# Kernel optimization log

Hardware: AMD Instinct MI355X
Metric: run time of the kernel (lower is better)

## Reference

```python
import jax, jax.numpy as jnp
import numpy as np

B, T, H = 8, 1024, 640
N_PHONE, N_PHONEME = 230, 96


def _make_mapping():
    # 0/1 phone->phoneme allophone map, shape (n_phoneme, n_phone).
    # Every phone maps to >=1 phoneme; every phoneme covered (n_phone > n_phoneme).
    rng = np.random.default_rng(0)
    m = np.zeros((N_PHONEME, N_PHONE), dtype=np.float32)
    cols = np.arange(N_PHONE)
    m[cols % N_PHONEME, cols] = 1.0
    m[rng.integers(0, N_PHONEME, size=N_PHONE), cols] = 1.0  # some phones are allophones of 2 phonemes
    m[0, 0] = 1.0  # blank -> blank, as in allophone_layer
    return jnp.asarray(m)


def setup_inputs() -> dict:
    key = jax.random.key(0)
    k1, k2 = jax.random.split(key)
    enc_output = jax.random.normal(k1, (B, T, H), dtype=jnp.float32)
    feature2phone = jax.random.normal(k2, (H, N_PHONE), dtype=jnp.float32)
    return {"enc_output": enc_output, "feature2phone": feature2phone, "mapping": _make_mapping()}


def reference(enc_output, feature2phone, mapping):
    # phone logits: (B,T,H) @ (H,P) -> (B,T,P), scaled by sqrt(H)
    hidden = feature2phone.shape[0]
    phone = jnp.einsum('bth,hp->btp', enc_output, feature2phone) / jnp.sqrt(jnp.asarray(hidden, enc_output.dtype))
    # broadcast-multiply with 0/1 map -> (B,T,M,P), mask zeros with -inf
    allo = phone[:, :, None, :] * mapping  # mapping: (M,P)
    allo = jnp.where(mapping > 0, allo, -jnp.inf)
    # masked max segment-reduce over the phone axis -> (B,T,M)
    phoneme = jnp.max(allo, axis=-1)
    # log-softmax over phoneme dim
    return jax.nn.log_softmax(phoneme, axis=2)
```

## Files before the change

kernel.cpp:

```cpp
#include <hip/hip_runtime.h>
#include <math.h>

#define NH 640
#define NP 230
#define NM 96
#define NROWS 8192
#define MAXL 32
#define NSTEP 20
#define MBLK 32
#define NBLOCKS (NROWS / MBLK)
#define PFB 14

#define OFF_CNT  0
#define OFF_CSR  4096
#define OFF_B    65536

typedef __bf16 bf16_t;
typedef bf16_t bf16x8 __attribute__((ext_vector_type(8)));
typedef float floatx4 __attribute__((ext_vector_type(4)));

static __device__ __forceinline__ unsigned short f2b(float f) {
    unsigned u = __float_as_uint(f);
    u += 0x7fffu + ((u >> 16) & 1u);
    return (unsigned short)(u >> 16);
}

__global__ __launch_bounds__(256)
void prep_kernel(const float* __restrict__ f2p,
                 const float* __restrict__ mapping,
                 int* __restrict__ cnt, int* __restrict__ csr,
                 unsigned short* __restrict__ wsB2) {
    const int b = blockIdx.x;
    const int tid = threadIdx.x;
    if (b < 24) {
        int wave = b * 4 + (tid >> 6);
        int lane = tid & 63;
        if (wave >= NM) return;
        int base = 0;
        #pragma unroll
        for (int c = 0; c < 4; ++c) {
            int p = c * 64 + lane;
            float v = (p < NP) ? mapping[wave * NP + p] : 0.0f;
            unsigned long long mask = __ballot(v > 0.0f);
            if (v > 0.0f) {
                int idx = base + __popcll(mask & ((1ull << lane) - 1ull));
                if (idx < MAXL) csr[wave * MAXL + idx] = p;
            }
            base += __popcll(mask);
        }
        if (lane == 0) cnt[wave] = base < MAXL ? base : MAXL;
    } else {
        int g = (b - 24) * 256 + tid;
        int m16  = g & 15;
        int quad = (g >> 4) & 3;
        int ct   = (g >> 6) & 15;
        int s    = g >> 10;
        int n = ct * 16 + m16;
        int k0 = s * 32 + quad * 8;
        unsigned short v[8];
        #pragma unroll
        for (int j = 0; j < 8; ++j)
            v[j] = (n < NP) ? f2b(f2p[(size_t)(k0 + j) * NP + n]) : (unsigned short)0;
        *(uint4*)(wsB2 + (size_t)g * 8) = *(const uint4*)v;
    }
}

__global__ __launch_bounds__(512, 2)
void fused_phonetics_kernel(const float* __restrict__ enc,
                            const unsigned short* __restrict__ wsB2,
                            const int* __restrict__ cnt,
                            const int* __restrict__ csr,
                            float* __restrict__ out) {
    __shared__ __align__(16) unsigned short sA[2560 * 8];
    __shared__ int scnt[NM];
    __shared__ int scsr[NM * MAXL];
    float (*phone)[257] = (float (*)[257])sA;

    const int tid  = threadIdx.x;
    const int lane = tid & 63;
    const int wv   = tid >> 6;
    const int m16  = lane & 15;
    const int quad = lane >> 4;
    const int row0 = blockIdx.x * MBLK;

    int creg[6];
    #pragma unroll
    for (int j = 0; j < 6; ++j) creg[j] = csr[tid + j * 512];
    int cc = (tid < NM) ? cnt[tid] : 0;

    float4 areg0[5], areg1[5];
    #pragma unroll
    for (int i = 0; i < 5; ++i) {
        int G = i * 8192 + tid * 16;
        int row = G / 1280;
        int cb4 = (G - row * 1280) >> 2;
        areg0[i] = *(const float4*)(enc + (size_t)(row0 + row) * NH + cb4);
    }
    #pragma unroll
    for (int i = 0; i < 5; ++i) {
        int G = i * 8192 + tid * 16;
        int row = G / 1280;
        int cb4 = (G - row * 1280) >> 2;
        areg1[i] = *(const float4*)(enc + (size_t)(row0 + row) * NH + 320 + cb4);
    }

    const unsigned short* bptr = wsB2 + ((size_t)(wv * 2) * 64 + lane) * 8;
    uint4 bpre[2 * NSTEP];
    #pragma unroll
    for (int s = 0; s < PFB; ++s) {
        bpre[2 * s + 0] = *(const uint4*)(bptr + ((size_t)s * 16 + 0) * 64 * 8);
        bpre[2 * s + 1] = *(const uint4*)(bptr + ((size_t)s * 16 + 1) * 64 * 8);
    }

    #pragma unroll
    for (int j = 0; j < 6; ++j) scsr[tid + j * 512] = creg[j];
    if (tid < NM) scnt[tid] = cc;

    #pragma unroll
    for (int i = 0; i < 5; ++i) {
        int G = i * 8192 + tid * 16;
        int row = G / 1280;
        int cb4 = (G - row * 1280) >> 2;
        int k = cb4;
        int s  = k >> 5;
        int q  = (k & 31) >> 3;
        int j0 = k & 7;
        unsigned short v[4];
        v[0] = f2b(areg0[i].x); v[1] = f2b(areg0[i].y);
        v[2] = f2b(areg0[i].z); v[3] = f2b(areg0[i].w);
        int soff = ((s * 2 + (row >> 4)) * 64 + q * 16 + (row & 15)) * 8 + j0;
        *(uint2*)(sA + soff) = *(const uint2*)v;
    }
    __syncthreads();

    #pragma unroll
    for (int s = PFB; s < NSTEP; ++s) {
        bpre[2 * s + 0] = *(const uint4*)(bptr + ((size_t)s * 16 + 0) * 64 * 8);
        bpre[2 * s + 1] = *(const uint4*)(bptr + ((size_t)s * 16 + 1) * 64 * 8);
    }

    floatx4 acc00 = {0.f,0.f,0.f,0.f}, acc01 = acc00, acc10 = acc00, acc11 = acc00;
    const unsigned short* aptr = sA + (size_t)lane * 8;

    #pragma unroll
    for (int s = 0; s < 10; ++s) {
        uint4 a0 = *(const uint4*)(aptr + (size_t)(s * 2 + 0) * 64 * 8);
        uint4 a1 = *(const uint4*)(aptr + (size_t)(s * 2 + 1) * 64 * 8);
        bf16x8 A0 = __builtin_bit_cast(bf16x8, a0);
        bf16x8 A1 = __builtin_bit_cast(bf16x8, a1);
        bf16x8 B0 = __builtin_bit_cast(bf16x8, bpre[2 * s + 0]);
        bf16x8 B1 = __builtin_bit_cast(bf16x8, bpre[2 * s + 1]);
        acc00 = __builtin_amdgcn_mfma_f32_16x16x32_bf16(A0, B0, acc00, 0, 0, 0);
        acc01 = __builtin_amdgcn_mfma_f32_16x16x32_bf16(A0, B1, acc01, 0, 0, 0);
        acc10 = __builtin_amdgcn_mfma_f32_16x16x32_bf16(A1, B0, acc10, 0, 0, 0);
        acc11 = __builtin_amdgcn_mfma_f32_16x16x32_bf16(A1, B1, acc11, 0, 0, 0);
    }

    #pragma unroll
    for (int i = 0; i < 5; ++i) {
        int G = i * 8192 + tid * 16;
        int row = G / 1280;
        int cb4 = (G - row * 1280) >> 2;
        int k = 320 + cb4;
        int s  = k >> 5;
        int q  = (k & 31) >> 3;
        int j0 = k & 7;
        unsigned short v[4];
        v[0] = f2b(areg1[i].x); v[1] = f2b(areg1[i].y);
        v[2] = f2b(areg1[i].z); v[3] = f2b(areg1[i].w);
        int soff = ((s * 2 + (row >> 4)) * 64 + q * 16 + (row & 15)) * 8 + j0;
        *(uint2*)(sA + soff) = *(const uint2*)v;
    }
    __syncthreads();

    #pragma unroll
    for (int s = 10; s < NSTEP; ++s) {
        uint4 a0 = *(const uint4*)(aptr + (size_t)(s * 2 + 0) * 64 * 8);
        uint4 a1 = *(const uint4*)(aptr + (size_t)(s * 2 + 1) * 64 * 8);
        bf16x8 A0 = __builtin_bit_cast(bf16x8, a0);
        bf16x8 A1 = __builtin_bit_cast(bf16x8, a1);
        bf16x8 B0 = __builtin_bit_cast(bf16x8, bpre[2 * s + 0]);
        bf16x8 B1 = __builtin_bit_cast(bf16x8, bpre[2 * s + 1]);
        acc00 = __builtin_amdgcn_mfma_f32_16x16x32_bf16(A0, B0, acc00, 0, 0, 0);
        acc01 = __builtin_amdgcn_mfma_f32_16x16x32_bf16(A0, B1, acc01, 0, 0, 0);
        acc10 = __builtin_amdgcn_mfma_f32_16x16x32_bf16(A1, B0, acc10, 0, 0, 0);
        acc11 = __builtin_amdgcn_mfma_f32_16x16x32_bf16(A1, B1, acc11, 0, 0, 0);
    }

    __syncthreads();

    const float scale = 0.03952847075210474f;
    #pragma unroll
    for (int i = 0; i < 4; ++i) {
        int r = quad * 4 + i;
        phone[r     ][wv * 32 +  0 + m16] = acc00[i] * scale;
        phone[r     ][wv * 32 + 16 + m16] = acc01[i] * scale;
        phone[r + 16][wv * 32 +  0 + m16] = acc10[i] * scale;
        phone[r + 16][wv * 32 + 16 + m16] = acc11[i] * scale;
    }
    __syncthreads();

    const int r   = tid >> 4;
    const int l16 = tid & 15;
    float pmv[6];
    float mx = -INFINITY;
    #pragma unroll
    for (int j = 0; j < 6; ++j) {
        int m = l16 + j * 16;
        int c = scnt[m];
        const int* lst = scsr + m * MAXL;
        float best = -INFINITY;
        for (int jj = 0; jj < c; ++jj) best = fmaxf(best, phone[r][lst[jj]]);
        pmv[j] = best;
        mx = fmaxf(mx, best);
    }
    #pragma unroll
    for (int d = 1; d < 16; d <<= 1) mx = fmaxf(mx, __shfl_xor(mx, d));
    float s = 0.f;
    #pragma unroll
    for (int j = 0; j < 6; ++j) s += __expf(pmv[j] - mx);
    #pragma unroll
    for (int d = 1; d < 16; d <<= 1) s += __shfl_xor(s, d);
    const float lse = mx + __logf(s);
    #pragma unroll
    for (int j = 0; j < 6; ++j)
        out[(size_t)(row0 + r) * NM + l16 + j * 16] = pmv[j] - lse;
}

extern "C" void kernel_launch(void* const* d_in, const int* in_sizes, int n_in,
                              void* d_out, int out_size, void* d_ws, size_t ws_size,
                              hipStream_t stream) {
    const float* enc     = (const float*)d_in[0];
    const float* f2p     = (const float*)d_in[1];
    const float* mapping = (const float*)d_in[2];
    float* out = (float*)d_out;

    char* ws = (char*)d_ws;
    int* cnt = (int*)(ws + OFF_CNT);
    int* csr = (int*)(ws + OFF_CSR);
    unsigned short* wsB2 = (unsigned short*)(ws + OFF_B);

    prep_kernel<<<104, 256, 0, stream>>>(f2p, mapping, cnt, csr, wsB2);
    fused_phonetics_kernel<<<NBLOCKS, 512, 0, stream>>>(enc, wsB2, cnt, csr, out);
}
```

Before: 80.82 us.

## Merge prep into main kernel with global atomic flag spin-wait

Removes the separate prep kernel: each of the 256 blocks now converts its share of the weight fragments to bf16, and the first 96 blocks also build the CSR mapping lists. Completion is signalled through an agent-scope atomic counter that every block spins on before loading B. The enc loads and the first LDS staging happen before the wait, so global load latency can overlap the cross-block prep. The aim is to save a kernel launch plus the gap between kernels. In exchange it adds a memset, relies on all 256 blocks being co-resident to avoid deadlock, and can no longer prefetch B ahead of the barrier.

```diff
diff --git a/kernel.cpp b/kernel.cpp
--- a/kernel.cpp
+++ b/kernel.cpp
@@ -9,9 +9,11 @@
 #define NSTEP 20
 #define MBLK 32
 #define NBLOCKS (NROWS / MBLK)
-#define PFB 14
-
-#define OFF_CNT  0
+#define FRAGS_PER_BLK 80
+#define FLAG_TARGET 608u
+
+#define OFF_FLAG 0
+#define OFF_CNT  512
 #define OFF_CSR  4096
 #define OFF_B    65536
 
@@ -25,52 +27,21 @@
     return (unsigned short)(u >> 16);
 }
 
-__global__ __launch_bounds__(256)
-void prep_kernel(const float* __restrict__ f2p,
-                 const float* __restrict__ mapping,
-                 int* __restrict__ cnt, int* __restrict__ csr,
-                 unsigned short* __restrict__ wsB2) {
-    const int b = blockIdx.x;
-    const int tid = threadIdx.x;
-    if (b < 24) {
-        int wave = b * 4 + (tid >> 6);
-        int lane = tid & 63;
-        if (wave >= NM) return;
-        int base = 0;
-        #pragma unroll
-        for (int c = 0; c < 4; ++c) {
-            int p = c * 64 + lane;
-            float v = (p < NP) ? mapping[wave * NP + p] : 0.0f;
-            unsigned long long mask = __ballot(v > 0.0f);
-            if (v > 0.0f) {
-                int idx = base + __popcll(mask & ((1ull << lane) - 1ull));
-                if (idx < MAXL) csr[wave * MAXL + idx] = p;
-            }
-            base += __popcll(mask);
-        }
-        if (lane == 0) cnt[wave] = base < MAXL ? base : MAXL;
-    } else {
-        int g = (b - 24) * 256 + tid;
-        int m16  = g & 15;
-        int quad = (g >> 4) & 3;
-        int ct   = (g >> 6) & 15;
-        int s    = g >> 10;
-        int n = ct * 16 + m16;
-        int k0 = s * 32 + quad * 8;
-        unsigned short v[8];
-        #pragma unroll
-        for (int j = 0; j < 8; ++j)
-            v[j] = (n < NP) ? f2b(f2p[(size_t)(k0 + j) * NP + n]) : (unsigned short)0;
-        *(uint4*)(wsB2 + (size_t)g * 8) = *(const uint4*)v;
-    }
+static __device__ __forceinline__ void lds_barrier() {
+    asm volatile("s_waitcnt lgkmcnt(0)" ::: "memory");
+    __builtin_amdgcn_s_barrier();
+    __builtin_amdgcn_sched_barrier(0);
 }
 
 __global__ __launch_bounds__(512, 2)
-void fused_phonetics_kernel(const float* __restrict__ enc,
-                            const unsigned short* __restrict__ wsB2,
-                            const int* __restrict__ cnt,
-                            const int* __restrict__ csr,
-                            float* __restrict__ out) {
+void fused_all_kernel(const float* __restrict__ enc,
+                      const float* __restrict__ f2p,
+                      const float* __restrict__ mapping,
+                      unsigned short* __restrict__ wsB2,
+                      int* __restrict__ cnt,
+                      int* __restrict__ csr,
+                      unsigned int* __restrict__ flag,
+                      float* __restrict__ out) {
     __shared__ __align__(16) unsigned short sA[2560 * 8];
     __shared__ int scnt[NM];
     __shared__ int scsr[NM * MAXL];
@@ -81,12 +52,49 @@
     const int wv   = tid >> 6;
     const int m16  = lane & 15;
     const int quad = lane >> 4;
-    const int row0 = blockIdx.x * MBLK;
-
-    int creg[6];
-    #pragma unroll
-    for (int j = 0; j < 6; ++j) creg[j] = csr[tid + j * 512];
-    int cc = (tid < NM) ? cnt[tid] : 0;
+    const int b    = blockIdx.x;
+    const int row0 = b * MBLK;
+
+    if (wv < 2) {
+        int t = wv * 64 + lane;
+        if (t < FRAGS_PER_BLK) {
+            int pg = b * FRAGS_PER_BLK + t;
+            int m16p = pg & 15;
+            int qd   = (pg >> 4) & 3;
+            int ct   = (pg >> 6) & 15;
+            int sp   = pg >> 10;
+            int pn = ct * 16 + m16p;
+            int k0 = sp * 32 + qd * 8;
+            unsigned short v[8];
+            #pragma unroll
+            for (int j = 0; j < 8; ++j)
+                v[j] = (pn < NP) ? f2b(f2p[(size_t)(k0 + j) * NP + pn]) : (unsigned short)0;
+            *(uint4*)(wsB2 + (size_t)pg * 8) = *(const uint4*)v;
+        }
+        if (lane == 0)
+            __hip_atomic_fetch_add(flag, 1u, __ATOMIC_RELEASE, __HIP_MEMORY_SCOPE_AGENT);
+    } else if (wv == 2 && b < NM) {
+        float mvv[4];
+        #pragma unroll
+        for (int c = 0; c < 4; ++c) {
+            int p = c * 64 + lane;
+            mvv[c] = (p < NP) ? mapping[b * NP + p] : 0.0f;
+        }
+        int base = 0;
+        #pragma unroll
+        for (int c = 0; c < 4; ++c) {
+            unsigned long long mask = __ballot(mvv[c] > 0.0f);
+            if (mvv[c] > 0.0f) {
+                int idx = base + __popcll(mask & ((1ull << lane) - 1ull));
+                if (idx < MAXL) csr[b * MAXL + idx] = c * 64 + lane;
+            }
+            base += __popcll(mask);
+        }
+        if (lane == 0) {
+            cnt[b] = base < MAXL ? base : MAXL;
+            __hip_atomic_fetch_add(flag, 1u, __ATOMIC_RELEASE, __HIP_MEMORY_SCOPE_AGENT);
+        }
+    }
 
     float4 areg0[5], areg1[5];
     #pragma unroll
@@ -103,18 +111,6 @@
         int cb4 = (G - row * 1280) >> 2;
         areg1[i] = *(const float4*)(enc + (size_t)(row0 + row) * NH + 320 + cb4);
     }
-
-    const unsigned short* bptr = wsB2 + ((size_t)(wv * 2) * 64 + lane) * 8;
-    uint4 bpre[2 * NSTEP];
-    #pragma unroll
-    for (int s = 0; s < PFB; ++s) {
-        bpre[2 * s + 0] = *(const uint4*)(bptr + ((size_t)s * 16 + 0) * 64 * 8);
-        bpre[2 * s + 1] = *(const uint4*)(bptr + ((size_t)s * 16 + 1) * 64 * 8);
-    }
-
-    #pragma unroll
-    for (int j = 0; j < 6; ++j) scsr[tid + j * 512] = creg[j];
-    if (tid < NM) scnt[tid] = cc;
 
     #pragma unroll
     for (int i = 0; i < 5; ++i) {
@@ -131,13 +127,28 @@
         int soff = ((s * 2 + (row >> 4)) * 64 + q * 16 + (row & 15)) * 8 + j0;
         *(uint2*)(sA + soff) = *(const uint2*)v;
     }
-    __syncthreads();
-
-    #pragma unroll
-    for (int s = PFB; s < NSTEP; ++s) {
+    lds_barrier();
+
+    while (__hip_atomic_load(flag, __ATOMIC_RELAXED, __HIP_MEMORY_SCOPE_AGENT) < FLAG_TARGET)
+        __builtin_amdgcn_s_sleep(2);
+    (void)__hip_atomic_load(flag, __ATOMIC_ACQUIRE, __HIP_MEMORY_SCOPE_AGENT);
+
+    int creg[6];
+    #pragma unroll
+    for (int j = 0; j < 6; ++j) creg[j] = csr[tid + j * 512];
+    int cc = (tid < NM) ? cnt[tid] : 0;
+
+    const unsigned short* bptr = wsB2 + ((size_t)(wv * 2) * 64 + lane) * 8;
+    uint4 bpre[2 * NSTEP];
+    #pragma unroll
+    for (int s = 0; s < NSTEP; ++s) {
         bpre[2 * s + 0] = *(const uint4*)(bptr + ((size_t)s * 16 + 0) * 64 * 8);
         bpre[2 * s + 1] = *(const uint4*)(bptr + ((size_t)s * 16 + 1) * 64 * 8);
     }
+
+    #pragma unroll
+    for (int j = 0; j < 6; ++j) scsr[tid + j * 512] = creg[j];
+    if (tid < NM) scnt[tid] = cc;
 
     floatx4 acc00 = {0.f,0.f,0.f,0.f}, acc01 = acc00, acc10 = acc00, acc11 = acc00;
     const unsigned short* aptr = sA + (size_t)lane * 8;
@@ -171,7 +182,7 @@
         int soff = ((s * 2 + (row >> 4)) * 64 + q * 16 + (row & 15)) * 8 + j0;
         *(uint2*)(sA + soff) = *(const uint2*)v;
     }
-    __syncthreads();
+    lds_barrier();
 
     #pragma unroll
     for (int s = 10; s < NSTEP; ++s) {
@@ -236,10 +247,11 @@
     float* out = (float*)d_out;
 
     char* ws = (char*)d_ws;
+    unsigned int* flag = (unsigned int*)(ws + OFF_FLAG);
     int* cnt = (int*)(ws + OFF_CNT);
     int* csr = (int*)(ws + OFF_CSR);
     unsigned short* wsB2 = (unsigned short*)(ws + OFF_B);
 
-    prep_kernel<<<104, 256, 0, stream>>>(f2p, mapping, cnt, csr, wsB2);
-    fused_phonetics_kernel<<<NBLOCKS, 512, 0, stream>>>(enc, wsB2, cnt, csr, out);
-}
+    hipMemsetAsync(ws + OFF_FLAG, 0, 4, stream);
+    fused_all_kernel<<<NBLOCKS, 512, 0, stream>>>(enc, f2p, mapping, wsB2, cnt, csr, flag, out);
+}
```

New measurement: 122.2 us. +51.2%, slower.
